# Kernel tuning notes

Measured on AMD Instinct MI355X. Metric: run time of the kernel, lower is better.

The kernel has to match this reference:

```python
import jax, jax.numpy as jnp
import numpy as np

B, N, E = 2, 32768, 32768
DIM = 3
MP_STEPS = 2
H = 32  # hidden width; original bug: depth == hidden width (range(hidden))


def _ln(x, g, b):
    m = jnp.mean(x, axis=-1, keepdims=True)
    v = jnp.var(x, axis=-1, keepdims=True)
    return (x - m) * jax.lax.rsqrt(v + 1e-5) * g + b


def _mlp(x, Win, bin_, Wh, bh, Wout, bout, lng=None, lnb=None):
    # Linear -> ReLU -> [LN] -> H x (Linear -> ReLU -> [LN]) -> Linear -> ReLU
    h = jax.nn.relu(x @ Win + bin_)
    if lng is not None:
        h = _ln(h, lng[0], lnb[0])
        def body(h, p):
            W, b_, g_, bb = p
            return _ln(jax.nn.relu(h @ W + b_), g_, bb), None
        h, _ = jax.lax.scan(body, h, (Wh, bh, lng[1:], lnb[1:]))
    else:
        def body(h, p):
            W, b_ = p
            return jax.nn.relu(h @ W + b_), None
        h, _ = jax.lax.scan(body, h, (Wh, bh))
    return jax.nn.relu(h @ Wout + bout)


def _mk(key, din, h, dout, ln, pref):
    ks = jax.random.split(key, 3)
    d = {
        pref + 'Win': jax.random.normal(ks[0], (din, h), jnp.float32) / np.sqrt(din).astype(np.float32),
        pref + 'bin': jnp.zeros((h,), jnp.float32),
        pref + 'Wh': jax.random.normal(ks[1], (h, h, h), jnp.float32) / np.sqrt(h).astype(np.float32),
        pref + 'bh': jnp.zeros((h, h), jnp.float32),
        pref + 'Wout': jax.random.normal(ks[2], (h, dout), jnp.float32) / np.sqrt(h).astype(np.float32),
        pref + 'bout': jnp.zeros((dout,), jnp.float32),
    }
    if ln:
        d[pref + 'lng'] = jnp.ones((h + 1, h), jnp.float32)
        d[pref + 'lnb'] = jnp.zeros((h + 1, h), jnp.float32)
    return d


def setup_inputs() -> dict:
    key = jax.random.key(0)
    ks = jax.random.split(key, 10)
    inp = {
        'nodes': jax.random.normal(ks[0], (B, N, 6), jnp.float32),
        'edges': jax.random.normal(ks[1], (B, E, 1), jnp.float32),
        'gvec': jax.random.normal(ks[2], (B,), jnp.float32),
        'senders': jax.random.randint(ks[3], (B, E), 0, N, jnp.int32),
        'receivers': jax.random.randint(ks[4], (B, E), 0, N, jnp.int32),
    }
    inp.update(_mk(ks[5], 6 + 1, H, 16, False, 'ne_'))          # node encoder: node_dim+global
    inp.update(_mk(ks[6], 1 + DIM + 1, H, 16, False, 'ed_'))    # edge encoder: edge_dim+dim+1
    inp.update(_mk(ks[7], 16 + 2 * 16 + 1, H, 16, True, 'pe_')) # edge processor
    inp.update(_mk(ks[8], 16 + 16 + 1, H, 16, True, 'pv_'))     # node processor
    inp.update(_mk(ks[9], 16, H, DIM, False, 'de_'))            # decoder
    return inp


def reference(nodes, edges, gvec, senders, receivers,
              ne_Win, ne_bin, ne_Wh, ne_bh, ne_Wout, ne_bout,
              ed_Win, ed_bin, ed_Wh, ed_bh, ed_Wout, ed_bout,
              pe_Win, pe_bin, pe_Wh, pe_bh, pe_Wout, pe_bout, pe_lng, pe_lnb,
              pv_Win, pv_bin, pv_Wh, pv_bh, pv_Wout, pv_bout, pv_lng, pv_lnb,
              de_Win, de_bin, de_Wh, de_bh, de_Wout, de_bout):
    g_node = jnp.broadcast_to(gvec[:, None, None], (B, N, 1))  # global repeated per node
    g_edge = jnp.broadcast_to(gvec[:, None, None], (B, E, 1))  # global repeated per edge
    x = jnp.concatenate([nodes, g_node], axis=-1)  # [B,N,7]

    # relative edge features from sender/receiver positions (first DIM cols)
    pos = x[..., :DIM]
    si = senders[:, :, None]
    ri = receivers[:, :, None]
    rel = jnp.take_along_axis(pos, si, axis=1) - jnp.take_along_axis(pos, ri, axis=1)  # [B,E,3]
    nrm = jnp.linalg.norm(rel, axis=-1, keepdims=True)
    e_in = jnp.concatenate([edges, rel, nrm], axis=-1)  # [B,E,5]

    ve = _mlp(x, ne_Win, ne_bin, ne_Wh, ne_bh, ne_Wout, ne_bout)       # [B,N,16]
    ee = _mlp(e_in, ed_Win, ed_bin, ed_Wh, ed_bh, ed_Wout, ed_bout)    # [B,E,16]

    seg = jax.vmap(lambda e, r: jax.ops.segment_sum(e, r, num_segments=N))

    for _ in range(MP_STEPS):
        # phi_e: gather sender/receiver node states, concat, edge MLP
        vs = jnp.take_along_axis(ve, si, axis=1)  # [B,E,16]
        vr = jnp.take_along_axis(ve, ri, axis=1)
        ee = _mlp(jnp.concatenate([ee, vs, vr, g_edge], axis=-1),
                  pe_Win, pe_bin, pe_Wh, pe_bh, pe_Wout, pe_bout, pe_lng, pe_lnb)
        # phi_v: scatter-add edge states into receiver nodes, concat, node MLP
        agg = seg(ee, receivers)  # [B,N,16]
        ve = _mlp(jnp.concatenate([agg, ve, g_node], axis=-1),
                  pv_Win, pv_bin, pv_Wh, pv_bh, pv_Wout, pv_bout, pv_lng, pv_lnb)

    return _mlp(ve, de_Win, de_bin, de_Wh, de_bh, de_Wout, de_bout)  # [B,N,3]
```

## Files before the change

kernel.cpp:

```cpp
#include <hip/hip_runtime.h>

#define BB 2
#define NN 32768
#define EN 32768

typedef unsigned int u32;
typedef __attribute__((ext_vector_type(8)))  short bf16x8;
typedef __attribute__((ext_vector_type(2)))  float f32x2;
typedef __attribute__((ext_vector_type(16))) float f32x16;

union U4 { uint4 u; bf16x8 h; };

__device__ __forceinline__ u32 pk2(float lo, float hi) {
    u32 r;
    asm("v_cvt_pk_bf16_f32 %0, %1, %2" : "=v"(r) : "v"(lo), "v"(hi));
    return r;
}

__device__ __forceinline__ float xor32_sum(float x) {
    float y = x;
    asm("v_permlane32_swap_b32 %0, %1" : "+v"(x), "+v"(y));
    return x + y;
}

__device__ __forceinline__ f32x16 MF32(bf16x8 a, bf16x8 b, f32x16 c) {
    return __builtin_amdgcn_mfma_f32_32x32x16_bf16(a, b, c, 0, 0, 0);
}

template<bool LN>
__device__ __forceinline__ void transform32(f32x16 D, bf16x8& B0, bf16x8& B1)
{
    f32x2 p0 = {D[0],D[1]},  p1 = {D[2],D[3]},  p2 = {D[4],D[5]},  p3 = {D[6],D[7]};
    f32x2 p4 = {D[8],D[9]},  p5 = {D[10],D[11]},p6 = {D[12],D[13]},p7 = {D[14],D[15]};
    const f32x2 zz = {0.f, 0.f};
    p0 = __builtin_elementwise_max(p0, zz); p1 = __builtin_elementwise_max(p1, zz);
    p2 = __builtin_elementwise_max(p2, zz); p3 = __builtin_elementwise_max(p3, zz);
    p4 = __builtin_elementwise_max(p4, zz); p5 = __builtin_elementwise_max(p5, zz);
    p6 = __builtin_elementwise_max(p6, zz); p7 = __builtin_elementwise_max(p7, zz);
    if (LN) {
        f32x2 sv = ((p0+p1)+(p2+p3)) + ((p4+p5)+(p6+p7));
        f32x2 ta = __builtin_elementwise_fma(p0,p0,
                   __builtin_elementwise_fma(p1,p1,
                   __builtin_elementwise_fma(p2,p2, p3*p3)));
        f32x2 tb = __builtin_elementwise_fma(p4,p4,
                   __builtin_elementwise_fma(p5,p5,
                   __builtin_elementwise_fma(p6,p6, p7*p7)));
        f32x2 tv = ta + tb;
        float s = xor32_sum(sv.x + sv.y);
        float t = xor32_sum(tv.x + tv.y);
        float mu  = s * (1.f/32.f);
        float var = fmaf(-mu, mu, t * (1.f/32.f));
        float rs  = rsqrtf(var + 1e-5f);
        float nt  = -mu * rs;
        f32x2 rs2 = {rs, rs}, nt2 = {nt, nt};
        p0 = __builtin_elementwise_fma(p0, rs2, nt2);
        p1 = __builtin_elementwise_fma(p1, rs2, nt2);
        p2 = __builtin_elementwise_fma(p2, rs2, nt2);
        p3 = __builtin_elementwise_fma(p3, rs2, nt2);
        p4 = __builtin_elementwise_fma(p4, rs2, nt2);
        p5 = __builtin_elementwise_fma(p5, rs2, nt2);
        p6 = __builtin_elementwise_fma(p6, rs2, nt2);
        p7 = __builtin_elementwise_fma(p7, rs2, nt2);
    }
    U4 c;
    c.u.x = pk2(p0.x,p0.y); c.u.y = pk2(p1.x,p1.y);
    c.u.z = pk2(p2.x,p2.y); c.u.w = pk2(p3.x,p3.y);
    B0 = c.h;
    c.u.x = pk2(p4.x,p4.y); c.u.y = pk2(p5.x,p5.y);
    c.u.z = pk2(p6.x,p6.y); c.u.w = pk2(p7.x,p7.y);
    B1 = c.h;
}

__device__ __forceinline__ f32x16 load_biasC(const float* WB, int base, int h) {
    return *(const f32x16*)(WB + base + h*16);
}

template<int NT, bool LN>
__device__ __forceinline__ f32x16 mlp32(const bf16x8* bIn,
    const u32* WL, const float* WB, int lane, int h)
{
    constexpr int HB = NT*256;
    constexpr int BO = HB + 16384;
    U4 c;
    f32x16 D = load_biasC(WB, 0, h);
    #pragma unroll
    for (int t = 0; t < NT; ++t) {
        c.u = *(const uint4*)(WL + t*256 + lane*4);
        D = MF32(c.h, bIn[t], D);
    }
    c.u = *(const uint4*)(WL + HB + lane*4);        bf16x8 w0 = c.h;
    c.u = *(const uint4*)(WL + HB + 256 + lane*4);  bf16x8 w1 = c.h;
    c.u = *(const uint4*)(WL + HB + 512 + lane*4);  bf16x8 x0 = c.h;
    c.u = *(const uint4*)(WL + HB + 768 + lane*4);  bf16x8 x1 = c.h;
    f32x16 pb = load_biasC(WB, 32, h);
    bf16x8 B0, B1;
    transform32<LN>(D, B0, B1);
    #pragma unroll 8
    for (int l = 0; l < 32; ++l) {
        const int lp = (l+2 < 32) ? l+2 : 31;
        c.u = *(const uint4*)(WL + HB + lp*512 + lane*4);       bf16x8 nw0 = c.h;
        c.u = *(const uint4*)(WL + HB + lp*512 + 256 + lane*4); bf16x8 nw1 = c.h;
        const int lb_ = (l+1 < 32) ? l+1 : 31;
        f32x16 nb = load_biasC(WB, 32 + lb_*32, h);
        __builtin_amdgcn_s_setprio(1);
        f32x16 E = MF32(w0, B0, pb);
        E = MF32(w1, B1, E);
        __builtin_amdgcn_s_setprio(0);
        transform32<LN>(E, B0, B1);
        w0 = x0; w1 = x1; x0 = nw0; x1 = nw1; pb = nb;
    }
    c.u = *(const uint4*)(WL + BO + lane*4);        bf16x8 o0 = c.h;
    c.u = *(const uint4*)(WL + BO + 256 + lane*4);  bf16x8 o1 = c.h;
    f32x16 Co = load_biasC(WB, 1056, h);
    __builtin_amdgcn_s_setprio(1);
    f32x16 O = MF32(o0, B0, Co);
    O = MF32(o1, B1, O);
    __builtin_amdgcn_s_setprio(0);
    return O;
}

__device__ __forceinline__ void stage_dma(u32* WL, const u32* __restrict__ Wp,
                                          int wtot, int tid, int nthr)
{
    const int lane = tid & 63;
    const int step = (nthr >> 6) * 256;
    for (int C = (tid >> 6)*256; C < wtot; C += step)
        __builtin_amdgcn_global_load_lds(
            (const __attribute__((address_space(1))) u32*)(Wp + C + lane*4),
            (__attribute__((address_space(3))) u32*)(WL + C), 16, 0, 0);
}

__device__ __forceinline__ void stage_bias(float* WB,
    const float* __restrict__ bin, const float* __restrict__ bhid,
    const float* __restrict__ bo, int nbo, int tid, int nthr)
{
    for (int i = tid; i < 1088; i += nthr) {
        float v;
        if (i < 32) {
            int w = i, hh = w>>4, r = w&15;
            int f = (r&3) + 8*(r>>2) + 4*hh;
            v = bin[f];
        } else if (i < 1056) {
            int l = (i-32)>>5, w = (i-32)&31, hh = w>>4, r = w&15;
            int f = (r&3) + 8*(r>>2) + 4*hh;
            v = bhid[l*32 + f];
        } else {
            int w = i-1056, hh = w>>4, r = w&15;
            int f = (r&3) + 8*(r>>2) + 4*hh;
            v = (f < nbo) ? bo[f] : 0.f;
        }
        WB[i] = v;
    }
}

__device__ __forceinline__ void stage_weights32(
    u32* WL, float* WB, const u32* __restrict__ Wp,
    const float* __restrict__ bin, const float* __restrict__ bhid,
    const float* __restrict__ bo, int wtot, int nbo, int tid, int nthr)
{
    stage_dma(WL, Wp, wtot, tid, nthr);
    stage_bias(WB, bin, bhid, bo, nbo, tid, nthr);
    __syncthreads();
}

__device__ __forceinline__ void pack_body32(
    const float* __restrict__ Win, const float* __restrict__ Wh,
    const float* __restrict__ Wout, const float* __restrict__ lng,
    u32* __restrict__ dst, int din, int dout, int NT, int lb, int tid)
{
    int t = lb * 256 + tid;
    int binW = NT * 256;
    int tot = binW + 16384 + 512;
    if (t >= tot) return;
    float lo, hi;
    if (t < binW) {
        int tt = t>>8, rem = t&255, ln_ = rem>>2, d = rem&3;
        int hh = ln_>>5, m = ln_&31;
        int f0 = 16*tt + 4*hh + 2*(d&1) + 8*(d>>1);
        lo = (f0   < din) ? Win[f0*32 + m]     : 0.f;
        hi = (f0+1 < din) ? Win[(f0+1)*32 + m] : 0.f;
    } else if (t < binW + 16384) {
        int u = t - binW, l = u>>9, v = u&511;
        int tt = v>>8, rem = v&255, ln_ = rem>>2, d = rem&3;
        int hh = ln_>>5, m = ln_&31;
        int f0 = 16*tt + 4*hh + 2*(d&1) + 8*(d>>1);
        lo = Wh[l*1024 + f0*32 + m];
        hi = Wh[l*1024 + (f0+1)*32 + m];
        if (lng) { lo *= lng[l*32 + f0]; hi *= lng[l*32 + f0 + 1]; }
    } else {
        int u = t - binW - 16384;
        int tt = u>>8, rem = u&255, ln_ = rem>>2, d = rem&3;
        int hh = ln_>>5, m = ln_&31;
        int f0 = 16*tt + 4*hh + 2*(d&1) + 8*(d>>1);
        lo = (m < dout) ? Wout[f0*dout + m]     : 0.f;
        hi = (m < dout) ? Wout[(f0+1)*dout + m] : 0.f;
        if (lng) { lo *= lng[1024 + f0]; hi *= lng[1024 + f0 + 1]; }
    }
    dst[t] = pk2(lo, hi);
}

__device__ __forceinline__ void fold_body(
    const float* __restrict__ Wh,   const float* __restrict__ bh,
    const float* __restrict__ Wout, const float* __restrict__ bout,
    const float* __restrict__ lnb,  float* __restrict__ fb, int lb, int tid)
{
    int j = lb * 256 + tid;
    if (j < 1024) {
        int l = j >> 5, jj = j & 31;
        float acc = bh[j];
        #pragma unroll
        for (int k = 0; k < 32; ++k)
            acc = fmaf(lnb[l*32 + k], Wh[l*1024 + k*32 + jj], acc);
        fb[j] = acc;
    } else if (j < 1024 + 16) {
        int jj = j - 1024;
        float acc = bout[jj];
        #pragma unroll
        for (int k = 0; k < 32; ++k)
            acc = fmaf(lnb[1024 + k], Wout[k*16 + jj], acc);
        fb[j] = acc;
    }
}

__global__ __launch_bounds__(256) void prep_kernel(
    const float* ne_Win, const float* ne_Wh, const float* ne_Wout,
    const float* ed_Win, const float* ed_Wh, const float* ed_Wout,
    const float* pe_Win, const float* pe_Wh, const float* pe_Wout,
    const float* pe_lng, const float* pe_lnb, const float* pe_bh, const float* pe_bout,
    const float* pe_bin,
    const float* pv_Win, const float* pv_Wh, const float* pv_Wout,
    const float* pv_lng, const float* pv_lnb, const float* pv_bh, const float* pv_bout,
    const float* pv_bin,
    const float* de_Win, const float* de_Wh, const float* de_Wout,
    const float* gvec,
    u32* Wne, u32* Wed, u32* Wpe, u32* Wpv, u32* Wde,
    float* Fpe, float* Fpv)
{
    int bx = blockIdx.x, tid = threadIdx.x;
    if      (bx < 67)  pack_body32(ne_Win, ne_Wh, ne_Wout, nullptr, Wne,  7, 16, 1, bx,       tid);
    else if (bx < 134) pack_body32(ed_Win, ed_Wh, ed_Wout, nullptr, Wed,  5, 16, 1, bx - 67,  tid);
    else if (bx < 203) pack_body32(pe_Win, pe_Wh, pe_Wout, pe_lng,  Wpe, 48, 16, 3, bx - 134, tid);
    else if (bx < 271) pack_body32(pv_Win, pv_Wh, pv_Wout, pv_lng,  Wpv, 32, 16, 2, bx - 203, tid);
    else if (bx < 338) pack_body32(de_Win, de_Wh, de_Wout, nullptr, Wde, 16,  3, 1, bx - 271, tid);
    else if (bx < 343) fold_body(pe_Wh, pe_bh, pe_Wout, pe_bout, pe_lnb, Fpe, bx - 338, tid);
    else if (bx < 348) fold_body(pv_Wh, pv_bh, pv_Wout, pv_bout, pv_lnb, Fpv, bx - 343, tid);
    else {
        if (tid < 64) {
            int b = tid >> 5, f = tid & 31;
            Fpe[1040 + tid] = pe_bin[f] + gvec[b] * pe_Win[48*32 + f];
        } else if (tid < 128) {
            int u = tid - 64, b = u >> 5, f = u & 31;
            Fpv[1040 + u] = pv_bin[f] + gvec[b] * pv_Win[32*32 + f];
        }
    }
}

__device__ __forceinline__ bf16x8 stage_chunk(const float* __restrict__ arr,
                                              size_t e, int h)
{
    const int off = h*4;
    float4 a = *(const float4*)(arr + e*16 + off);
    float4 b = *(const float4*)(arr + e*16 + off + 8);
    U4 c;
    c.u.x = pk2(a.x, a.y); c.u.y = pk2(a.z, a.w);
    c.u.z = pk2(b.x, b.y); c.u.w = pk2(b.z, b.w);
    return c.h;
}

#define WAVE_SETUP \
    const int lane = threadIdx.x & 63; \
    const int wid  = threadIdx.x >> 6; \
    const int el = lane & 31, h = lane >> 5;

__global__ __launch_bounds__(512, 4) void encode_kernel(
    const float* __restrict__ nodes, const float* __restrict__ edges,
    const float* __restrict__ gvec,
    const int* __restrict__ senders, const int* __restrict__ receivers,
    const u32* __restrict__ Wne, const float* __restrict__ ne_bin,
    const float* __restrict__ ne_bh, const float* __restrict__ ne_bout,
    const u32* __restrict__ Wed, const float* __restrict__ ed_bin,
    const float* __restrict__ ed_bh, const float* __restrict__ ed_bout,
    u32* __restrict__ veB, u32* __restrict__ eeB)
{
    __shared__ __align__(64) u32 SL[17152 + 1088];
    u32* WL = SL;
    float* WB = (float*)(SL + 17152);
    WAVE_SETUP
    const bool edge_stage = blockIdx.x >= 256;
    stage_weights32(WL, WB,
                    edge_stage ? Wed : Wne,
                    edge_stage ? ed_bin : ne_bin,
                    edge_stage ? ed_bh : ne_bh,
                    edge_stage ? ed_bout : ne_bout,
                    17152, 16, threadIdx.x, 512);
    const int lb = edge_stage ? (blockIdx.x - 256) : blockIdx.x;
    const int e = (lb*8 + wid)*32 + el;
    const int b = e >> 15;
    bf16x8 a0;
    {
        uint4 w; w.x = 0u; w.y = 0u; w.z = 0u; w.w = 0u;
        if (!edge_stage) {
            if (h == 0) {
                float2 v01 = *(const float2*)(nodes + (size_t)e*6);
                float2 v23 = *(const float2*)(nodes + (size_t)e*6 + 2);
                w.x = pk2(v01.x, v01.y); w.y = pk2(v23.x, v23.y);
            } else {
                float2 v45 = *(const float2*)(nodes + (size_t)e*6 + 4);
                w.x = pk2(v45.x, v45.y); w.y = pk2(gvec[b], 0.f);
            }
        } else {
            int s = senders[e], r = receivers[e];
            const float* ps = nodes + ((size_t)b*NN + s)*6;
            const float* pr = nodes + ((size_t)b*NN + r)*6;
            float2 s01 = *(const float2*)ps; float s2v = ps[2];
            float2 r01 = *(const float2*)pr; float r2v = pr[2];
            float r0 = s01.x - r01.x, r1 = s01.y - r01.y, r2 = s2v - r2v;
            if (h == 0) {
                w.x = pk2(edges[e], r0); w.y = pk2(r1, r2);
            } else {
                w.x = pk2(sqrtf(r0*r0 + r1*r1 + r2*r2), 0.f);
            }
        }
        U4 c; c.u = w; a0 = c.h;
    }
    u32* dstB = edge_stage ? eeB : veB;
    f32x16 O = mlp32<1, false>(&a0, WL, WB, lane, h);
    U4 cc;
    cc.u.x = pk2(fmaxf(O[0],0.f), fmaxf(O[1],0.f));
    cc.u.y = pk2(fmaxf(O[2],0.f), fmaxf(O[3],0.f));
    cc.u.z = pk2(fmaxf(O[4],0.f), fmaxf(O[5],0.f));
    cc.u.w = pk2(fmaxf(O[6],0.f), fmaxf(O[7],0.f));
    *(uint4*)(dstB + (size_t)e*8 + h*4) = cc.u;
}

__global__ __launch_bounds__(512, 2) void edge_update_kernel(
    const int* __restrict__ senders, const int* __restrict__ receivers,
    const u32* __restrict__ veB, u32* __restrict__ eeB, float* __restrict__ agg,
    const u32* __restrict__ Wp, const float* __restrict__ F)
{
    __shared__ __align__(64) u32 SL[17664 + 1088 + 8*544];
    u32* WL = SL;
    float* WB = (float*)(SL + 17664);
    WAVE_SETUP
    float* X = (float*)(SL + 18752) + wid*544;
    const float* binSel = F + 1040 + ((blockIdx.x & 128) ? 32 : 0);
    stage_weights32(WL, WB, Wp, binSel, F, F + 1024, 17664, 16, threadIdx.x, 512);
    const int e0 = (blockIdx.x*8 + wid)*32;
    const int e  = e0 + el;
    const int b  = e >> 15;
    const int s  = senders[e], r_ = receivers[e];
    bf16x8 a[3];
    U4 c;
    c.u = *(const uint4*)(eeB + (size_t)e*8 + h*4);               a[0] = c.h;
    c.u = *(const uint4*)(veB + ((size_t)b*NN + s )*8 + h*4);     a[1] = c.h;
    c.u = *(const uint4*)(veB + ((size_t)b*NN + r_)*8 + h*4);     a[2] = c.h;
    f32x16 O = mlp32<3, true>(a, WL, WB, lane, h);
    float4 s1, s2;
    s1.x = fmaxf(O[0], 0.f); s1.y = fmaxf(O[1], 0.f);
    s1.z = fmaxf(O[2], 0.f); s1.w = fmaxf(O[3], 0.f);
    s2.x = fmaxf(O[4], 0.f); s2.y = fmaxf(O[5], 0.f);
    s2.z = fmaxf(O[6], 0.f); s2.w = fmaxf(O[7], 0.f);
    U4 cc;
    cc.u.x = pk2(s1.x, s1.y); cc.u.y = pk2(s1.z, s1.w);
    cc.u.z = pk2(s2.x, s2.y); cc.u.w = pk2(s2.z, s2.w);
    *(uint4*)(eeB + (size_t)e*8 + h*4) = cc.u;
    *(float4*)(X + el*17 + h*4)     = s1;
    *(float4*)(X + el*17 + h*4 + 8) = s2;
    const int feat = lane & 15;
    #pragma unroll
    for (int rr = 0; rr < 8; ++rr) {
        int m = (lane >> 4)*8 + rr;
        float v = X[m*17 + feat];
        int rc = __shfl(r_, m);
        int eg = e0 + m;
        atomicAdd(agg + ((size_t)(eg >> 15)*NN + rc)*16 + feat, v);
    }
}

template<bool DEC>
__global__ __launch_bounds__(512, 2) void node_update_kernel(
    const float* __restrict__ agg, u32* __restrict__ veB,
    const u32* __restrict__ Wp, const float* __restrict__ F,
    const u32* __restrict__ Wde, const float* __restrict__ de_bin,
    const float* __restrict__ de_bh, const float* __restrict__ de_bout,
    float* __restrict__ out)
{
    __shared__ __align__(64) u32 SL[DEC ? (17408 + 17152 + 1088 + 1088) : (17408 + 1088)];
    u32* WL = SL;
    u32* WL2 = SL + 17408;
    float* WB  = (float*)(SL + (DEC ? 34560 : 17408));
    float* WB2 = (float*)(SL + 35648);
    WAVE_SETUP
    const float* binSel = F + 1040 + ((blockIdx.x & 128) ? 32 : 0);
    stage_weights32(WL, WB, Wp, binSel, F, F + 1024, 17408, 16, threadIdx.x, 512);
    if (DEC)
        stage_weights32(WL2, WB2, Wde, de_bin, de_bh, de_bout, 17152, 3,
                        threadIdx.x, 512);
    const int e = (blockIdx.x*8 + wid)*32 + el;
    const int b = e >> 15;
    bf16x8 a[2];
    a[0] = stage_chunk(agg, (size_t)e, h);
    {
        U4 c;
        c.u = *(const uint4*)(veB + (size_t)e*8 + h*4);
        a[1] = c.h;
    }
    f32x16 O = mlp32<2, true>(a, WL, WB, lane, h);
    if (!DEC) {
        U4 cc;
        cc.u.x = pk2(fmaxf(O[0],0.f), fmaxf(O[1],0.f));
        cc.u.y = pk2(fmaxf(O[2],0.f), fmaxf(O[3],0.f));
        cc.u.z = pk2(fmaxf(O[4],0.f), fmaxf(O[5],0.f));
        cc.u.w = pk2(fmaxf(O[6],0.f), fmaxf(O[7],0.f));
        *(uint4*)(veB + (size_t)e*8 + h*4) = cc.u;
    } else {
        bf16x8 D0, D1;
        transform32<false>(O, D0, D1);
        f32x16 O2 = mlp32<1, false>(&D0, WL2, WB2, lane, h);
        if (h == 0) {
            out[(size_t)e*3 + 0] = fmaxf(O2[0], 0.f);
            out[(size_t)e*3 + 1] = fmaxf(O2[1], 0.f);
            out[(size_t)e*3 + 2] = fmaxf(O2[2], 0.f);
        }
    }
}

extern "C" void kernel_launch(void* const* d_in, const int* in_sizes, int n_in,
                              void* d_out, int out_size, void* d_ws, size_t ws_size,
                              hipStream_t stream)
{
    const float* nodes     = (const float*)d_in[0];
    const float* edges     = (const float*)d_in[1];
    const float* gvec      = (const float*)d_in[2];
    const int*   senders   = (const int*)  d_in[3];
    const int*   receivers = (const int*)  d_in[4];

    const float* ne_Win  = (const float*)d_in[5];
    const float* ne_bin  = (const float*)d_in[6];
    const float* ne_Wh   = (const float*)d_in[7];
    const float* ne_bh   = (const float*)d_in[8];
    const float* ne_Wout = (const float*)d_in[9];
    const float* ne_bout = (const float*)d_in[10];

    const float* ed_Win  = (const float*)d_in[11];
    const float* ed_bin  = (const float*)d_in[12];
    const float* ed_Wh   = (const float*)d_in[13];
    const float* ed_bh   = (const float*)d_in[14];
    const float* ed_Wout = (const float*)d_in[15];
    const float* ed_bout = (const float*)d_in[16];

    const float* pe_Win  = (const float*)d_in[17];
    const float* pe_bin  = (const float*)d_in[18];
    const float* pe_Wh   = (const float*)d_in[19];
    const float* pe_bh   = (const float*)d_in[20];
    const float* pe_Wout = (const float*)d_in[21];
    const float* pe_bout = (const float*)d_in[22];
    const float* pe_lng  = (const float*)d_in[23];
    const float* pe_lnb  = (const float*)d_in[24];

    const float* pv_Win  = (const float*)d_in[25];
    const float* pv_bin  = (const float*)d_in[26];
    const float* pv_Wh   = (const float*)d_in[27];
    const float* pv_bh   = (const float*)d_in[28];
    const float* pv_Wout = (const float*)d_in[29];
    const float* pv_bout = (const float*)d_in[30];
    const float* pv_lng  = (const float*)d_in[31];
    const float* pv_lnb  = (const float*)d_in[32];

    const float* de_Win  = (const float*)d_in[33];
    const float* de_bin  = (const float*)d_in[34];
    const float* de_Wh   = (const float*)d_in[35];
    const float* de_bh   = (const float*)d_in[36];
    const float* de_Wout = (const float*)d_in[37];
    const float* de_bout = (const float*)d_in[38];

    float* ve   = (float*)d_ws;
    float* ee   = ve   + (size_t)1048576;
    float* agg0 = ee   + (size_t)1048576;
    float* agg1 = agg0 + (size_t)1048576;
    u32* veB = (u32*)ve;
    u32* eeB = (u32*)ee;
    u32* Wne = (u32*)(agg1 + (size_t)1048576);
    u32* Wed = Wne + 17152;
    u32* Wpe = Wed + 17152;
    u32* Wpv = Wpe + 17664;
    u32* Wde = Wpv + 17408;
    float* Fpe = (float*)(Wde + 17152);
    float* Fpv = Fpe + 1104;

    prep_kernel<<<349, dim3(256), 0, stream>>>(
        ne_Win, ne_Wh, ne_Wout,
        ed_Win, ed_Wh, ed_Wout,
        pe_Win, pe_Wh, pe_Wout, pe_lng, pe_lnb, pe_bh, pe_bout, pe_bin,
        pv_Win, pv_Wh, pv_Wout, pv_lng, pv_lnb, pv_bh, pv_bout, pv_bin,
        de_Win, de_Wh, de_Wout, gvec,
        Wne, Wed, Wpe, Wpv, Wde, Fpe, Fpv);

    hipMemsetAsync(agg0, 0, (size_t)2 * 1048576 * sizeof(float), stream);

    encode_kernel<<<512, dim3(512), 0, stream>>>(nodes, edges, gvec, senders, receivers,
        Wne, ne_bin, ne_bh, ne_bout,
        Wed, ed_bin, ed_bh, ed_bout, veB, eeB);

    edge_update_kernel<<<256, dim3(512), 0, stream>>>(senders, receivers,
        veB, eeB, agg0, Wpe, Fpe);
    node_update_kernel<false><<<256, dim3(512), 0, stream>>>(agg0, veB,
        Wpv, Fpv, Wde, de_bin, de_bh, de_bout, (float*)d_out);
    edge_update_kernel<<<256, dim3(512), 0, stream>>>(senders, receivers,
        veB, eeB, agg1, Wpe, Fpe);
    node_update_kernel<true><<<256, dim3(512), 0, stream>>>(agg1, veB,
        Wpv, Fpv, Wde, de_bin, de_bh, de_bout, (float*)d_out);
}
```

Before: 231.6 us.

## Aggregate edge messages with packed bf16 atomics instead of fp32 atomics

The scatter-add of edge states into receiver nodes now uses global_atomic_pk_add_bf16 into a bf16 aggregation buffer. This halves atomic traffic and the memset size, and the node update reads bf16 pairs directly instead of converting fp32. The LDS transpose buffer is re-laid out with stride 18 for float2 reads. The hidden-layer loop also drops its prefetch index clamps and unrolls 16, so it reads weights and biases past the last layer. Summing in bf16 loses precision, and concurrent low-precision adds may accumulate rounding error.

```diff
diff --git a/kernel.cpp b/kernel.cpp
--- a/kernel.cpp
+++ b/kernel.cpp
@@ -21,6 +21,11 @@
     float y = x;
     asm("v_permlane32_swap_b32 %0, %1" : "+v"(x), "+v"(y));
     return x + y;
+}
+
+__device__ __forceinline__ void atomic_pk_bf16(u32* addr, u32 data) {
+    asm volatile("global_atomic_pk_add_bf16 %0, %1, off"
+                 :: "v"(addr), "v"(data) : "memory");
 }
 
 __device__ __forceinline__ f32x16 MF32(bf16x8 a, bf16x8 b, f32x16 c) {
@@ -95,13 +100,11 @@
     f32x16 pb = load_biasC(WB, 32, h);
     bf16x8 B0, B1;
     transform32<LN>(D, B0, B1);
-    #pragma unroll 8
+    #pragma unroll 16
     for (int l = 0; l < 32; ++l) {
-        const int lp = (l+2 < 32) ? l+2 : 31;
-        c.u = *(const uint4*)(WL + HB + lp*512 + lane*4);       bf16x8 nw0 = c.h;
-        c.u = *(const uint4*)(WL + HB + lp*512 + 256 + lane*4); bf16x8 nw1 = c.h;
-        const int lb_ = (l+1 < 32) ? l+1 : 31;
-        f32x16 nb = load_biasC(WB, 32 + lb_*32, h);
+        c.u = *(const uint4*)(WL + HB + (l+2)*512 + lane*4);       bf16x8 nw0 = c.h;
+        c.u = *(const uint4*)(WL + HB + (l+2)*512 + 256 + lane*4); bf16x8 nw1 = c.h;
+        f32x16 nb = load_biasC(WB, 32 + (l+1)*32, h);
         __builtin_amdgcn_s_setprio(1);
         f32x16 E = MF32(w0, B0, pb);
         E = MF32(w1, B1, E);
@@ -253,18 +256,6 @@
             Fpv[1040 + u] = pv_bin[f] + gvec[b] * pv_Win[32*32 + f];
         }
     }
-}
-
-__device__ __forceinline__ bf16x8 stage_chunk(const float* __restrict__ arr,
-                                              size_t e, int h)
-{
-    const int off = h*4;
-    float4 a = *(const float4*)(arr + e*16 + off);
-    float4 b = *(const float4*)(arr + e*16 + off + 8);
-    U4 c;
-    c.u.x = pk2(a.x, a.y); c.u.y = pk2(a.z, a.w);
-    c.u.z = pk2(b.x, b.y); c.u.w = pk2(b.z, b.w);
-    return c.h;
 }
 
 #define WAVE_SETUP \
@@ -335,14 +326,14 @@
 
 __global__ __launch_bounds__(512, 2) void edge_update_kernel(
     const int* __restrict__ senders, const int* __restrict__ receivers,
-    const u32* __restrict__ veB, u32* __restrict__ eeB, float* __restrict__ agg,
+    const u32* __restrict__ veB, u32* __restrict__ eeB, u32* __restrict__ aggB,
     const u32* __restrict__ Wp, const float* __restrict__ F)
 {
-    __shared__ __align__(64) u32 SL[17664 + 1088 + 8*544];
+    __shared__ __align__(64) u32 SL[17664 + 1088 + 8*576];
     u32* WL = SL;
     float* WB = (float*)(SL + 17664);
     WAVE_SETUP
-    float* X = (float*)(SL + 18752) + wid*544;
+    float* X = (float*)(SL + 18752) + wid*576;
     const float* binSel = F + 1040 + ((blockIdx.x & 128) ? 32 : 0);
     stage_weights32(WL, WB, Wp, binSel, F, F + 1024, 17664, 16, threadIdx.x, 512);
     const int e0 = (blockIdx.x*8 + wid)*32;
@@ -364,22 +355,22 @@
     cc.u.x = pk2(s1.x, s1.y); cc.u.y = pk2(s1.z, s1.w);
     cc.u.z = pk2(s2.x, s2.y); cc.u.w = pk2(s2.z, s2.w);
     *(uint4*)(eeB + (size_t)e*8 + h*4) = cc.u;
-    *(float4*)(X + el*17 + h*4)     = s1;
-    *(float4*)(X + el*17 + h*4 + 8) = s2;
-    const int feat = lane & 15;
+    *(float4*)(X + el*18 + h*4)     = s1;
+    *(float4*)(X + el*18 + h*4 + 8) = s2;
+    const int pw = lane & 7;
     #pragma unroll
-    for (int rr = 0; rr < 8; ++rr) {
-        int m = (lane >> 4)*8 + rr;
-        float v = X[m*17 + feat];
+    for (int rr = 0; rr < 4; ++rr) {
+        int m = (lane >> 3) + rr*8;
+        float2 v = *(const float2*)(X + m*18 + 2*pw);
+        u32 d = pk2(v.x, v.y);
         int rc = __shfl(r_, m);
-        int eg = e0 + m;
-        atomicAdd(agg + ((size_t)(eg >> 15)*NN + rc)*16 + feat, v);
+        atomic_pk_bf16(aggB + ((size_t)b*NN + rc)*8 + pw, d);
     }
 }
 
 template<bool DEC>
 __global__ __launch_bounds__(512, 2) void node_update_kernel(
-    const float* __restrict__ agg, u32* __restrict__ veB,
+    const u32* __restrict__ aggB, u32* __restrict__ veB,
     const u32* __restrict__ Wp, const float* __restrict__ F,
     const u32* __restrict__ Wde, const float* __restrict__ de_bin,
     const float* __restrict__ de_bh, const float* __restrict__ de_bout,
@@ -397,11 +388,13 @@
         stage_weights32(WL2, WB2, Wde, de_bin, de_bh, de_bout, 17152, 3,
                         threadIdx.x, 512);
     const int e = (blockIdx.x*8 + wid)*32 + el;
-    const int b = e >> 15;
     bf16x8 a[2];
-    a[0] = stage_chunk(agg, (size_t)e, h);
     {
         U4 c;
+        uint2 q1 = *(const uint2*)(aggB + (size_t)e*8 + 2*h);
+        uint2 q2 = *(const uint2*)(aggB + (size_t)e*8 + 2*h + 4);
+        c.u.x = q1.x; c.u.y = q1.y; c.u.z = q2.x; c.u.w = q2.y;
+        a[0] = c.h;
         c.u = *(const uint4*)(veB + (size_t)e*8 + h*4);
         a[1] = c.h;
     }
@@ -474,13 +467,11 @@
     const float* de_Wout = (const float*)d_in[37];
     const float* de_bout = (const float*)d_in[38];
 
-    float* ve   = (float*)d_ws;
-    float* ee   = ve   + (size_t)1048576;
-    float* agg0 = ee   + (size_t)1048576;
-    float* agg1 = agg0 + (size_t)1048576;
-    u32* veB = (u32*)ve;
-    u32* eeB = (u32*)ee;
-    u32* Wne = (u32*)(agg1 + (size_t)1048576);
+    u32* veB   = (u32*)d_ws;
+    u32* eeB   = veB   + (size_t)524288;
+    u32* agg0B = eeB   + (size_t)524288;
+    u32* agg1B = agg0B + (size_t)524288;
+    u32* Wne = agg1B + (size_t)524288;
     u32* Wed = Wne + 17152;
     u32* Wpe = Wed + 17152;
     u32* Wpv = Wpe + 17664;
@@ -496,18 +487,18 @@
         de_Win, de_Wh, de_Wout, gvec,
         Wne, Wed, Wpe, Wpv, Wde, Fpe, Fpv);
 
-    hipMemsetAsync(agg0, 0, (size_t)2 * 1048576 * sizeof(float), stream);
+    hipMemsetAsync(agg0B, 0, (size_t)2 * 524288 * sizeof(u32), stream);
 
     encode_kernel<<<512, dim3(512), 0, stream>>>(nodes, edges, gvec, senders, receivers,
         Wne, ne_bin, ne_bh, ne_bout,
         Wed, ed_bin, ed_bh, ed_bout, veB, eeB);
 
     edge_update_kernel<<<256, dim3(512), 0, stream>>>(senders, receivers,
-        veB, eeB, agg0, Wpe, Fpe);
-    node_update_kernel<false><<<256, dim3(512), 0, stream>>>(agg0, veB,
+        veB, eeB, agg0B, Wpe, Fpe);
+    node_update_kernel<false><<<256, dim3(512), 0, stream>>>(agg0B, veB,
         Wpv, Fpv, Wde, de_bin, de_bh, de_bout, (float*)d_out);
     edge_update_kernel<<<256, dim3(512), 0, stream>>>(senders, receivers,
-        veB, eeB, agg1, Wpe, Fpe);
-    node_update_kernel<true><<<256, dim3(512), 0, stream>>>(agg1, veB,
+        veB, eeB, agg1B, Wpe, Fpe);
+    node_update_kernel<true><<<256, dim3(512), 0, stream>>>(agg1B, veB,
         Wpv, Fpv, Wde, de_bin, de_bh, de_bout, (float*)d_out);
 }
```

Result: no change. 234.2 us (+1.1%).
